# Kernel optimization log

Hardware: AMD Instinct MI355X
Metric: run time of the kernel (lower is better)

Reference implementation:

```python
import jax, jax.numpy as jnp
import numpy as np

N = 512          # n_nodes
F = 64           # hidden scalar/vector channels (hidden_irreps 64x0e+64x1o)
S = 5            # num_species
T = 32           # time embedding dim
M = 64           # MLP_irreps 64x0e
L = 2            # num_interactions
AVG = 511.0      # avg_num_neighbors (fully connected)
E = N * (N - 1)


def _sph(v):
    """Real spherical harmonics l=0,1,2 (component norm) of normalized vectors. v: [E,3]."""
    r = jnp.linalg.norm(v, axis=-1, keepdims=True)  # [E,1]
    u = v / r
    x, y, z = u[..., 0], u[..., 1], u[..., 2]
    s3, s5, s15 = 3.0 ** 0.5, 5.0 ** 0.5, 15.0 ** 0.5
    Y0 = jnp.ones_like(x)[..., None]
    Y1 = s3 * u
    Y2 = jnp.stack([s15 * x * y, s15 * y * z, 0.5 * s5 * (3 * z * z - 1.0),
                    s15 * x * z, 0.5 * s15 * (x * x - y * y)], axis=-1)
    return jnp.concatenate([Y0, Y1, Y2], axis=-1), r  # [E,9], [E,1]


def setup_inputs() -> dict:
    key = jax.random.key(0)
    ks = jax.random.split(key, 16)
    snd, rcv = np.nonzero(~np.eye(N, dtype=bool))  # fully-connected, no self loops
    return dict(
        positions=jax.random.normal(ks[0], (N, 3), jnp.float32),
        node_features=jax.random.randint(ks[1], (N,), 1, S + 1, jnp.int32),
        time_embedding=jax.random.normal(ks[2], (T,), jnp.float32),
        senders=jnp.asarray(snd, jnp.int32),
        receivers=jnp.asarray(rcv, jnp.int32),
        W_embed=jax.random.normal(ks[3], (S + T, F)) * 0.1,
        b_embed=jnp.zeros((F,)),
        W_lin=jax.random.normal(ks[4], (L, 3, F, F)) / jnp.sqrt(float(F)),
        W_e1=jax.random.normal(ks[5], (L, 1, 32)),
        b_e1=jnp.zeros((L, 32)),
        W_e2=jax.random.normal(ks[6], (L, 32, F * 6)) * 0.05,
        Wp0=jax.random.normal(ks[7], (L, S, F, 6)) * 0.1,
        Wp1=jax.random.normal(ks[8], (L, S, F, 3)) * 0.1,
        Wr1=jax.random.normal(ks[9], (L, F, M)) / jnp.sqrt(float(F)),
        br1=jnp.zeros((L, M)),
        Wr2s=jax.random.normal(ks[10], (L, M, 16)) * 0.1,
        Wr2g=jax.random.normal(ks[11], (L, M, F)) * 0.1,
    )


def reference(positions, node_features, time_embedding, senders, receivers,
              W_embed, b_embed, W_lin, W_e1, b_e1, W_e2, Wp0, Wp1, Wr1, br1, Wr2s, Wr2g):
    species = node_features - 1                                  # ints in [0,S)
    onehot = jax.nn.one_hot(species, S, dtype=positions.dtype)   # /normalization_factor=1
    te = jnp.tile(time_embedding, (N, 1))
    h = jnp.concatenate([onehot, te], axis=-1) @ W_embed + b_embed  # embedding Dense -> [N,F]
    node_feats = jnp.zeros((N, F, 9), positions.dtype).at[:, :, 0].set(h)
    pos0 = positions
    pos = positions
    for l in range(L):
        vec = pos[receivers] - pos[senders]                      # [E,3]
        Y, lengths = _sph(vec)                                   # SH of edge dirs, edge lengths
        # per-l channel-mixing linear on node feats
        x0 = jnp.einsum('nf,fg->ng', node_feats[:, :, 0], W_lin[l, 0])
        x1 = jnp.einsum('nfm,fg->ngm', node_feats[:, :, 1:4], W_lin[l, 1])
        x2 = jnp.einsum('nfm,fg->ngm', node_feats[:, :, 4:9], W_lin[l, 2])
        s0, s1, s2 = x0[senders], x1[senders], x2[senders]       # gather sender feats
        # edge-length MLP producing per-channel per-CG-path weights
        he = jax.nn.silu(lengths @ W_e1[l] + b_e1[l])            # [E,32]
        w = (he @ W_e2[l]).reshape(-1, F, 6)                     # 6 TP paths
        Y1 = Y[:, None, 1:4]
        Y2c = Y[:, None, 4:9]
        # CG tensor-product paths: 0x0->0, 0x1->1, 0x2->2, 1x1->0, 1x1->1, 2x2->0
        m0 = (w[..., 0] * s0 * Y[:, 0:1]
              + w[..., 3] * jnp.sum(s1 * Y1, -1)
              + w[..., 5] * jnp.sum(s2 * Y2c, -1))               # [E,F]
        m1 = w[..., 1, None] * s0[..., None] * Y1 + w[..., 4, None] * jnp.cross(s1, Y1)
        m2 = w[..., 2, None] * s0[..., None] * Y2c
        msg = jnp.concatenate([m0[..., None], m1, m2], axis=-1)  # [E,F,9]
        A = jax.ops.segment_sum(msg, receivers, num_segments=N) / AVG  # scatter-aggregate
        # EquivariantProductBasisBlock: species-weighted symmetric contractions (correlation 3)
        A0, A1, A2 = A[:, :, 0], A[:, :, 1:4], A[:, :, 4:9]
        n1 = jnp.sum(A1 * A1, -1)
        n2 = jnp.sum(A2 * A2, -1)
        t0 = jnp.stack([A0, A0 * A0, A0 ** 3, n1, n2, A0 * n1], axis=-1)
        w0 = Wp0[l][species]                                     # [N,F,6]
        w1 = Wp1[l][species]                                     # [N,F,3]
        out0 = jnp.sum(t0 * w0, -1)                              # [N,F] scalars
        gpoly = w1[..., 0] + w1[..., 1] * A0 + w1[..., 2] * A0 * A0
        out1 = gpoly[..., None] * A1                             # [N,F,3] vectors
        node_feats = (jnp.zeros((N, F, 9), positions.dtype)
                      .at[:, :, 0].set(out0).at[:, :, 1:4].set(out1))
        # NonLinearReadoutBlock: gated vector readout (scalar outputs are discarded upstream)
        hr = jax.nn.silu(out0 @ Wr1[l] + br1[l])
        gate = hr @ Wr2g[l]                                      # [N,F]
        vec_out = jnp.einsum('nf,nfc->nc', gate, out1)           # [N,3] many_body_vectors
        pos = pos + vec_out
    return (pos - pos0)[:, :3]                                    # final_scaling = 1.0
```

## Files before the change

### kernel.cpp

```cpp
#include <hip/hip_runtime.h>
#include <hip/hip_bf16.h>

using bf16 = __hip_bfloat16;
using bf16x8 = __attribute__((ext_vector_type(8))) short;
using f32x4  = __attribute__((ext_vector_type(4))) float;

#define NN 512
#define NS 511

enum : int {
  WS_FLAG = 0,
  WS_X0S  = 16,
  WS_POS  = 336,
  WS_POS2 = 1872,
  WS_DELTA= 3408,
  WS_XS1  = 4960,
};

__device__ __forceinline__ short f2b(float x) {
  unsigned u = __builtin_bit_cast(unsigned, x);
  unsigned r = (u + 0x7fffu + ((u >> 16) & 1u)) >> 16;
  return (short)r;
}

__device__ __forceinline__ float ld(const void* p, int i, int isf32) {
  if (isf32) return ((const float*)p)[i];
  return __bfloat162float(((const bf16*)p)[i]);
}

__global__ __launch_bounds__(320) void k_pre(
    const void* __restrict__ positions, const void* __restrict__ te,
    const void* __restrict__ W_embed, const void* __restrict__ b_embed,
    const void* __restrict__ W_lin, float* __restrict__ ws) {
  const int t = threadIdx.x;
  __shared__ int flag_s;
  __shared__ float hst[5][64];
  if (t < 64) {
    int cnt = 0;
    #pragma unroll
    for (int kq = 0; kq < 4; ++kq) {
      float v = __bfloat162float(((const bf16*)W_embed)[t + kq * 64]);
      float av = fabsf(v);
      cnt += (v == v && av > 1e-8f && av < 1e4f) ? 1 : 0;
    }
    #pragma unroll
    for (int off = 32; off > 0; off >>= 1) cnt += __shfl_down(cnt, off);
    if (t == 0) {
      int isf32 = (cnt >= 240) ? 0 : 1;
      flag_s = isf32;
      ((int*)ws)[WS_FLAG] = isf32;
    }
  }
  __syncthreads();
  const int isf32 = flag_s;
  for (int idx = t; idx < NN * 3; idx += 320)
    ws[WS_POS + idx] = ld(positions, idx, isf32);
  __shared__ float tv[64];
  if (t < 64) {
    float s = ld(b_embed, t, isf32);
    #pragma unroll 8
    for (int q = 0; q < 32; ++q)
      s += ld(te, q, isf32) * ld(W_embed, (5 + q) * 64 + t, isf32);
    tv[t] = s;
  }
  __syncthreads();
  {
    int sp = t >> 6, q = t & 63;
    hst[sp][q] = tv[q] + ld(W_embed, sp * 64 + q, isf32);
  }
  __syncthreads();
  {
    int sp = t >> 6, f = t & 63;
    float a0 = 0.f;
    #pragma unroll 8
    for (int q = 0; q < 64; ++q)
      a0 += hst[sp][q] * ld(W_lin, q * 64 + f, isf32);
    ws[WS_X0S + sp * 64 + f] = a0;
  }
}

template <int L>
__global__ __launch_bounds__(256) void k_edgenode(
    const int* __restrict__ nodef, const void* __restrict__ W_lin,
    const void* __restrict__ W_e1, const void* __restrict__ b_e1,
    const void* __restrict__ W_e2, const void* __restrict__ Wp0,
    const void* __restrict__ Wp1, const void* __restrict__ Wr1,
    const void* __restrict__ br1, const void* __restrict__ Wr2g,
    float* __restrict__ ws, void* __restrict__ out) {
  constexpr int HAS1 = L;
  constexpr int K = HAS1 ? 5 : 3;
  constexpr int N = K * 64;
  const int j = blockIdx.x;
  const int t = threadIdx.x;
  const int lane = t & 63;
  const int wave = t >> 6;
  const int quad = lane >> 4;
  const int lo = lane & 15;

  __shared__ short Bhi[N * 40];
  __shared__ float red[4][64][9];
  __shared__ float Af[64][9];
  __shared__ float s0l[64];
  __shared__ float o1l[3][64];
  __shared__ float hl[64];
  __shared__ float X0l[320];

  const int isf32 = ((const int*)ws)[WS_FLAG];

  {
    for (int idx = t; idx < N * 32; idx += 256) {
      int n = idx >> 5, h = idx & 31;
      int kp = n >> 6, f = n & 63;
      int src = (L * 32 + h) * 384 + f * 6 + kp;
      short bits;
      if (isf32) bits = f2b(((const float*)W_e2)[src]);
      else       bits = ((const short*)W_e2)[src];
      Bhi[n * 40 + h] = bits;
    }
    if (!HAS1) {
      for (int idx = t; idx < 320; idx += 256) X0l[idx] = ws[WS_X0S + idx];
    }
  }
  const float* pos = ws + (L ? WS_POS2 : WS_POS);
  const f32x4* xs = (const f32x4*)(ws + WS_XS1);
  float we1v[8], be1v[8];
  #pragma unroll
  for (int i = 0; i < 8; ++i) {
    we1v[i] = ld(W_e1, L * 32 + quad * 8 + i, isf32);
    be1v[i] = ld(b_e1, L * 32 + quad * 8 + i, isf32);
  }
  const float pjx = pos[j * 3 + 0], pjy = pos[j * 3 + 1], pjz = pos[j * 3 + 2];

  const float s3 = 1.7320508075688772f;
  const float s5h = 1.118033988749895f;
  const float s15 = 3.872983346207417f;
  const float s15h = 1.9364916731037085f;

  float acc[9][4] = {};
  __syncthreads();

  #pragma unroll 1
  for (int stile = wave; stile < 32; stile += 4) {
    bf16x8 af;
    {
      int ida = stile * 16 + lo;
      int ia = ida + (ida >= j);
      if (ia > 511) ia = 511;
      float pix = pos[ia * 3 + 0], piy = pos[ia * 3 + 1], piz = pos[ia * 3 + 2];
      float vx = pjx - pix, vy = pjy - piy, vz = pjz - piz;
      float r = sqrtf(vx * vx + vy * vy + vz * vz);
      #pragma unroll
      for (int i = 0; i < 8; ++i) {
        float x = r * we1v[i] + be1v[i];
        float he = x / (1.f + __expf(-x));
        af[i] = f2b(he);
      }
    }
    float Y1r[4][3], Y2r[4][5];
    int ir[4], sp4[4];
    bool vld[4];
    #pragma unroll
    for (int r4 = 0; r4 < 4; ++r4) {
      int idx = stile * 16 + quad * 4 + r4;
      vld[r4] = idx < NS;
      int i = idx + (idx >= j);
      if (i > 511) i = 511;
      ir[r4] = i;
      if (!HAS1) sp4[r4] = nodef[i] - 1;
      float pix = pos[i * 3 + 0], piy = pos[i * 3 + 1], piz = pos[i * 3 + 2];
      float vx = pjx - pix, vy = pjy - piy, vz = pjz - piz;
      float r2 = vx * vx + vy * vy + vz * vz;
      float rinv = r2 > 0.f ? rsqrtf(r2) : 0.f;
      float ux = vx * rinv, uy = vy * rinv, uz = vz * rinv;
      Y1r[r4][0] = s3 * ux; Y1r[r4][1] = s3 * uy; Y1r[r4][2] = s3 * uz;
      Y2r[r4][0] = s15 * ux * uy;
      Y2r[r4][1] = s15 * uy * uz;
      Y2r[r4][2] = s5h * (3.f * uz * uz - 1.f);
      Y2r[r4][3] = s15 * ux * uz;
      Y2r[r4][4] = s15h * (ux * ux - uy * uy);
    }
    #pragma unroll
    for (int ft = 0; ft < 4; ++ft) {
      int fcol = ft * 16 + lo;
      f32x4 xv[4];
      if (HAS1) {
        #pragma unroll
        for (int r4 = 0; r4 < 4; ++r4) xv[r4] = xs[ir[r4] * 64 + fcol];
      } else {
        #pragma unroll
        for (int r4 = 0; r4 < 4; ++r4) {
          f32x4 v = {X0l[sp4[r4] * 64 + fcol], 0.f, 0.f, 0.f};
          xv[r4] = v;
        }
      }
      f32x4 C[K];
      #pragma unroll
      for (int kp = 0; kp < K; ++kp) {
        const bf16x8 bh = *(const bf16x8*)&Bhi[(kp * 64 + fcol) * 40 + quad * 8];
        f32x4 c = {0.f, 0.f, 0.f, 0.f};
        C[kp] = __builtin_amdgcn_mfma_f32_16x16x32_bf16(af, bh, c, 0, 0, 0);
      }
      #pragma unroll
      for (int r4 = 0; r4 < 4; ++r4) {
        if (vld[r4]) {
          float s0 = xv[r4].x;
          float w0 = C[0][r4], w1 = C[1][r4], w2 = C[2][r4];
          if (HAS1) {
            float s1x = xv[r4].y, s1y = xv[r4].z, s1z = xv[r4].w;
            float w3 = C[3][r4], w4 = C[4][r4];
            float d1 = s1x * Y1r[r4][0] + s1y * Y1r[r4][1] + s1z * Y1r[r4][2];
            float cx = s1y * Y1r[r4][2] - s1z * Y1r[r4][1];
            float cy = s1z * Y1r[r4][0] - s1x * Y1r[r4][2];
            float cz = s1x * Y1r[r4][1] - s1y * Y1r[r4][0];
            acc[0][ft] += w0 * s0 + w3 * d1;
            float t1 = w1 * s0;
            acc[1][ft] += t1 * Y1r[r4][0] + w4 * cx;
            acc[2][ft] += t1 * Y1r[r4][1] + w4 * cy;
            acc[3][ft] += t1 * Y1r[r4][2] + w4 * cz;
          } else {
            acc[0][ft] += w0 * s0;
            float t1 = w1 * s0;
            acc[1][ft] += t1 * Y1r[r4][0];
            acc[2][ft] += t1 * Y1r[r4][1];
            acc[3][ft] += t1 * Y1r[r4][2];
          }
          float t2 = w2 * s0;
          acc[4][ft] += t2 * Y2r[r4][0];
          acc[5][ft] += t2 * Y2r[r4][1];
          acc[6][ft] += t2 * Y2r[r4][2];
          acc[7][ft] += t2 * Y2r[r4][3];
          acc[8][ft] += t2 * Y2r[r4][4];
        }
      }
    }
  }

  #pragma unroll
  for (int c = 0; c < 9; ++c)
    #pragma unroll
    for (int ft = 0; ft < 4; ++ft) {
      float v = acc[c][ft];
      v += __shfl_xor(v, 16);
      v += __shfl_xor(v, 32);
      acc[c][ft] = v;
    }
  if (quad == 0) {
    #pragma unroll
    for (int c = 0; c < 9; ++c)
      #pragma unroll
      for (int ft = 0; ft < 4; ++ft)
        red[wave][ft * 16 + lo][c] = acc[c][ft];
  }
  __syncthreads();
  for (int o = t; o < 576; o += 256) {
    int f = o / 9, c = o % 9;
    Af[f][c] = (red[0][f][c] + red[1][f][c] + red[2][f][c] + red[3][f][c]) *
               (1.f / 511.f);
  }
  __syncthreads();

  float out0 = 0.f, o1x = 0.f, o1y = 0.f, o1z = 0.f;
  if (t < 64) {
    int f = t;
    float a[9];
    #pragma unroll
    for (int c = 0; c < 9; ++c) a[c] = Af[f][c];
    int sp = nodef[j] - 1;
    int b0i = ((L * 5 + sp) * 64 + f) * 6;
    int b1i = ((L * 5 + sp) * 64 + f) * 3;
    float A0 = a[0];
    float n1 = a[1] * a[1] + a[2] * a[2] + a[3] * a[3];
    float n2 = a[4] * a[4] + a[5] * a[5] + a[6] * a[6] + a[7] * a[7] + a[8] * a[8];
    float A02 = A0 * A0;
    out0 = ld(Wp0, b0i + 0, isf32) * A0 + ld(Wp0, b0i + 1, isf32) * A02 +
           ld(Wp0, b0i + 2, isf32) * A02 * A0 + ld(Wp0, b0i + 3, isf32) * n1 +
           ld(Wp0, b0i + 4, isf32) * n2 + ld(Wp0, b0i + 5, isf32) * A0 * n1;
    float gp = ld(Wp1, b1i + 0, isf32) + ld(Wp1, b1i + 1, isf32) * A0 +
               ld(Wp1, b1i + 2, isf32) * A02;
    o1x = gp * a[1]; o1y = gp * a[2]; o1z = gp * a[3];
    s0l[f] = out0;
    if (L == 0) { o1l[0][f] = o1x; o1l[1][f] = o1y; o1l[2][f] = o1z; }
  }
  __syncthreads();
  if (t < 64) {
    int f = t;
    if (L == 0) {
      float b0 = 0.f, bx = 0.f, by = 0.f, bz = 0.f;
      #pragma unroll 8
      for (int q = 0; q < 64; ++q) {
        float w0 = ld(W_lin, 3 * 4096 + q * 64 + f, isf32);
        float w1 = ld(W_lin, 4 * 4096 + q * 64 + f, isf32);
        b0 += s0l[q] * w0;
        bx += o1l[0][q] * w1; by += o1l[1][q] * w1; bz += o1l[2][q] * w1;
      }
      f32x4 o = {b0, bx, by, bz};
      *(f32x4*)&ws[WS_XS1 + (j * 64 + f) * 4] = o;
    }
    float hacc = ld(br1, L * 64 + f, isf32);
    #pragma unroll 8
    for (int q = 0; q < 64; ++q)
      hacc += s0l[q] * ld(Wr1, (L * 64 + q) * 64 + f, isf32);
    hl[f] = hacc / (1.f + __expf(-hacc));
  }
  __syncthreads();
  if (t < 64) {
    int f = t;
    float gacc = 0.f;
    #pragma unroll 8
    for (int m = 0; m < 64; ++m)
      gacc += hl[m] * ld(Wr2g, (L * 64 + m) * 64 + f, isf32);
    float px = gacc * o1x, py = gacc * o1y, pz = gacc * o1z;
    #pragma unroll
    for (int off = 32; off > 0; off >>= 1) {
      px += __shfl_down(px, off);
      py += __shfl_down(py, off);
      pz += __shfl_down(pz, off);
    }
    if (f == 0) {
      if (L == 0) {
        ws[WS_DELTA + j * 3 + 0] = px;
        ws[WS_DELTA + j * 3 + 1] = py;
        ws[WS_DELTA + j * 3 + 2] = pz;
        ws[WS_POS2 + j * 3 + 0] = pos[j * 3 + 0] + px;
        ws[WS_POS2 + j * 3 + 1] = pos[j * 3 + 1] + py;
        ws[WS_POS2 + j * 3 + 2] = pos[j * 3 + 2] + pz;
      } else {
        float ox = ws[WS_DELTA + j * 3 + 0] + px;
        float oy = ws[WS_DELTA + j * 3 + 1] + py;
        float oz = ws[WS_DELTA + j * 3 + 2] + pz;
        if (isf32) {
          float* o = (float*)out;
          o[j * 3 + 0] = ox; o[j * 3 + 1] = oy; o[j * 3 + 2] = oz;
        } else {
          bf16* o = (bf16*)out;
          o[j * 3 + 0] = __float2bfloat16(ox);
          o[j * 3 + 1] = __float2bfloat16(oy);
          o[j * 3 + 2] = __float2bfloat16(oz);
        }
      }
    }
  }
}

extern "C" void kernel_launch(void* const* d_in, const int* in_sizes, int n_in,
                              void* d_out, int out_size, void* d_ws, size_t ws_size,
                              hipStream_t stream) {
  const void* positions = d_in[0];
  const int*  nodef     = (const int*)d_in[1];
  const void* te        = d_in[2];
  const void* W_embed   = d_in[5];
  const void* b_embed   = d_in[6];
  const void* W_lin     = d_in[7];
  const void* W_e1      = d_in[8];
  const void* b_e1      = d_in[9];
  const void* W_e2      = d_in[10];
  const void* Wp0       = d_in[11];
  const void* Wp1       = d_in[12];
  const void* Wr1       = d_in[13];
  const void* br1       = d_in[14];
  const void* Wr2g      = d_in[16];
  float* ws = (float*)d_ws;
  (void)in_sizes; (void)n_in; (void)out_size; (void)ws_size;

  k_pre<<<dim3(1), dim3(320), 0, stream>>>(positions, te, W_embed, b_embed,
                                           W_lin, ws);
  k_edgenode<0><<<dim3(512), dim3(256), 0, stream>>>(
      nodef, W_lin, W_e1, b_e1, W_e2, Wp0, Wp1, Wr1, br1, Wr2g, ws, d_out);
  k_edgenode<1><<<dim3(512), dim3(256), 0, stream>>>(
      nodef, W_lin, W_e1, b_e1, W_e2, Wp0, Wp1, Wr1, br1, Wr2g, ws, d_out);
}
```

Baseline: 194.0 us.

## Fuse preprocessing into layer-0 and factor layer-0 message sum by species

The single-block preprocessing kernel is merged into the layer-0 per-node kernel, so each block recomputes the embedding and positions into shared memory and one launch is removed. Layer 0 no longer runs the per-edge MFMA against W_e2. Because layer-0 sender features depend only on species, each block accumulates per-species sums of the radial hidden activations times the spherical harmonics (45x32 values). It then contracts these with W_e2 and the species embeddings once per node. This swaps per-edge matrix work for per-edge scalar FMAs, at the cost of redundant per-block setup and more registers.

Result: slower. 202.0 us (+4.1%).

```diff
diff --git a/kernel.cpp b/kernel.cpp
--- a/kernel.cpp
+++ b/kernel.cpp
@@ -28,13 +28,36 @@
   return __bfloat162float(((const bf16*)p)[i]);
 }
 
-__global__ __launch_bounds__(320) void k_pre(
-    const void* __restrict__ positions, const void* __restrict__ te,
-    const void* __restrict__ W_embed, const void* __restrict__ b_embed,
-    const void* __restrict__ W_lin, float* __restrict__ ws) {
+__global__ __launch_bounds__(256) void k_l0(
+    const void* __restrict__ positions, const int* __restrict__ nodef,
+    const void* __restrict__ te, const void* __restrict__ W_embed,
+    const void* __restrict__ b_embed, const void* __restrict__ W_lin,
+    const void* __restrict__ W_e1, const void* __restrict__ b_e1,
+    const void* __restrict__ W_e2, const void* __restrict__ Wp0,
+    const void* __restrict__ Wp1, const void* __restrict__ Wr1,
+    const void* __restrict__ br1, const void* __restrict__ Wr2g,
+    float* __restrict__ ws) {
+  const int j = blockIdx.x;
   const int t = threadIdx.x;
-  __shared__ int flag_s;
-  __shared__ float hst[5][64];
+  const int lane = t & 63;
+  const int wave = t >> 6;
+  const int h = lane & 31;
+  const int half = lane >> 5;
+
+  __shared__ int   flag_s;
+  __shared__ float posl[NN * 3];
+  __shared__ int   spl[NN];
+  __shared__ float we1s[32], be1s[32];
+  __shared__ float tv[64];
+  __shared__ float hstl[5][64];
+  __shared__ float X0Sl[5][64];
+  __shared__ float W2T[3][32][64];
+  __shared__ float Gred[4][45][32];
+  __shared__ float Af[64][9];
+  __shared__ float s0l[64];
+  __shared__ float o1l[3][64];
+  __shared__ float hl[64];
+
   if (t < 64) {
     int cnt = 0;
     #pragma unroll
@@ -46,16 +69,23 @@
     #pragma unroll
     for (int off = 32; off > 0; off >>= 1) cnt += __shfl_down(cnt, off);
     if (t == 0) {
-      int isf32 = (cnt >= 240) ? 0 : 1;
-      flag_s = isf32;
-      ((int*)ws)[WS_FLAG] = isf32;
+      int f32v = (cnt >= 240) ? 0 : 1;
+      flag_s = f32v;
+      if (j == 0) ((int*)ws)[WS_FLAG] = f32v;
     }
   }
   __syncthreads();
   const int isf32 = flag_s;
-  for (int idx = t; idx < NN * 3; idx += 320)
-    ws[WS_POS + idx] = ld(positions, idx, isf32);
-  __shared__ float tv[64];
+
+  for (int idx = t; idx < NN * 3; idx += 256) posl[idx] = ld(positions, idx, isf32);
+  for (int idx = t; idx < NN; idx += 256) spl[idx] = nodef[idx] - 1;
+  if (t < 32)      we1s[t]      = ld(W_e1, t, isf32);
+  else if (t < 64) be1s[t - 32] = ld(b_e1, t - 32, isf32);
+  for (int idx = t; idx < 3 * 32 * 64; idx += 256) {
+    int k = idx >> 11, rem = idx & 2047;
+    int hh = rem >> 6, f = rem & 63;
+    W2T[k][hh][f] = ld(W_e2, hh * 384 + f * 6 + k, isf32);
+  }
   if (t < 64) {
     float s = ld(b_embed, t, isf32);
     #pragma unroll 8
@@ -64,31 +94,172 @@
     tv[t] = s;
   }
   __syncthreads();
-  {
-    int sp = t >> 6, q = t & 63;
-    hst[sp][q] = tv[q] + ld(W_embed, sp * 64 + q, isf32);
-  }
-  __syncthreads();
-  {
-    int sp = t >> 6, f = t & 63;
+  for (int o = t; o < 320; o += 256) {
+    int sp = o >> 6, q = o & 63;
+    hstl[sp][q] = tv[q] + ld(W_embed, sp * 64 + q, isf32);
+  }
+  __syncthreads();
+  for (int o = t; o < 320; o += 256) {
+    int sp = o >> 6, f = o & 63;
     float a0 = 0.f;
     #pragma unroll 8
     for (int q = 0; q < 64; ++q)
-      a0 += hst[sp][q] * ld(W_lin, q * 64 + f, isf32);
-    ws[WS_X0S + sp * 64 + f] = a0;
+      a0 += hstl[sp][q] * ld(W_lin, q * 64 + f, isf32);
+    X0Sl[sp][f] = a0;
+  }
+  __syncthreads();
+
+  const float s3 = 1.7320508075688772f;
+  const float s5h = 1.118033988749895f;
+  const float s15 = 3.872983346207417f;
+  const float s15h = 1.9364916731037085f;
+
+  const float pjx = posl[j * 3 + 0], pjy = posl[j * 3 + 1], pjz = posl[j * 3 + 2];
+  const float we1h = we1s[h], be1h = be1s[h];
+
+  float G[45];
+  #pragma unroll
+  for (int c = 0; c < 45; ++c) G[c] = 0.f;
+
+  #pragma unroll 1
+  for (int it = 0; it < 64; ++it) {
+    int sidx = it * 8 + wave * 2 + half;
+    if (sidx < NS) {
+      int i = sidx + (sidx >= j);
+      float pix = posl[i * 3 + 0], piy = posl[i * 3 + 1], piz = posl[i * 3 + 2];
+      float vx = pjx - pix, vy = pjy - piy, vz = pjz - piz;
+      float r2 = vx * vx + vy * vy + vz * vz;
+      float rinv = r2 > 0.f ? rsqrtf(r2) : 0.f;
+      float r = r2 * rinv;
+      float ux = vx * rinv, uy = vy * rinv, uz = vz * rinv;
+      float x = r * we1h + be1h;
+      float he = x / (1.f + __expf(-x));
+      float Y1x = s3 * ux, Y1y = s3 * uy, Y1z = s3 * uz;
+      float Y2a = s15 * ux * uy, Y2b = s15 * uy * uz;
+      float Y2c = s5h * (3.f * uz * uz - 1.f);
+      float Y2d = s15 * ux * uz, Y2e = s15h * (ux * ux - uy * uy);
+      int sp = spl[i];
+      #pragma unroll
+      for (int spi = 0; spi < 5; ++spi) {
+        float hem = (sp == spi) ? he : 0.f;
+        G[spi * 9 + 0] += hem;
+        G[spi * 9 + 1] += hem * Y1x;
+        G[spi * 9 + 2] += hem * Y1y;
+        G[spi * 9 + 3] += hem * Y1z;
+        G[spi * 9 + 4] += hem * Y2a;
+        G[spi * 9 + 5] += hem * Y2b;
+        G[spi * 9 + 6] += hem * Y2c;
+        G[spi * 9 + 7] += hem * Y2d;
+        G[spi * 9 + 8] += hem * Y2e;
+      }
+    }
+  }
+
+  #pragma unroll
+  for (int c = 0; c < 45; ++c) G[c] += __shfl_xor(G[c], 32);
+  if (lane < 32) {
+    #pragma unroll
+    for (int c = 0; c < 45; ++c) Gred[wave][c][h] = G[c];
+  }
+  __syncthreads();
+  for (int o = t; o < 45 * 32; o += 256) {
+    int c = o >> 5, hh = o & 31;
+    Gred[0][c][hh] = Gred[0][c][hh] + Gred[1][c][hh] + Gred[2][c][hh] +
+                     Gred[3][c][hh];
+  }
+  __syncthreads();
+
+  for (int o = t; o < 576; o += 256) {
+    int f = o & 63, c = o >> 6;
+    int kc = (c == 0) ? 0 : (c < 4 ? 1 : 2);
+    float s = 0.f;
+    #pragma unroll
+    for (int sp = 0; sp < 5; ++sp) {
+      float d = 0.f;
+      #pragma unroll 8
+      for (int hh = 0; hh < 32; ++hh)
+        d += Gred[0][sp * 9 + c][hh] * W2T[kc][hh][f];
+      s += X0Sl[sp][f] * d;
+    }
+    Af[f][c] = s * (1.f / 511.f);
+  }
+  __syncthreads();
+
+  float out0 = 0.f, o1x = 0.f, o1y = 0.f, o1z = 0.f;
+  if (t < 64) {
+    int f = t;
+    float a[9];
+    #pragma unroll
+    for (int c = 0; c < 9; ++c) a[c] = Af[f][c];
+    int sp = nodef[j] - 1;
+    int b0i = (sp * 64 + f) * 6;
+    int b1i = (sp * 64 + f) * 3;
+    float A0 = a[0];
+    float n1 = a[1] * a[1] + a[2] * a[2] + a[3] * a[3];
+    float n2 = a[4] * a[4] + a[5] * a[5] + a[6] * a[6] + a[7] * a[7] + a[8] * a[8];
+    float A02 = A0 * A0;
+    out0 = ld(Wp0, b0i + 0, isf32) * A0 + ld(Wp0, b0i + 1, isf32) * A02 +
+           ld(Wp0, b0i + 2, isf32) * A02 * A0 + ld(Wp0, b0i + 3, isf32) * n1 +
+           ld(Wp0, b0i + 4, isf32) * n2 + ld(Wp0, b0i + 5, isf32) * A0 * n1;
+    float gp = ld(Wp1, b1i + 0, isf32) + ld(Wp1, b1i + 1, isf32) * A0 +
+               ld(Wp1, b1i + 2, isf32) * A02;
+    o1x = gp * a[1]; o1y = gp * a[2]; o1z = gp * a[3];
+    s0l[f] = out0;
+    o1l[0][f] = o1x; o1l[1][f] = o1y; o1l[2][f] = o1z;
+  }
+  __syncthreads();
+  if (t < 64) {
+    int f = t;
+    float b0 = 0.f, bx = 0.f, by = 0.f, bz = 0.f;
+    #pragma unroll 8
+    for (int q = 0; q < 64; ++q) {
+      float w0 = ld(W_lin, 3 * 4096 + q * 64 + f, isf32);
+      float w1 = ld(W_lin, 4 * 4096 + q * 64 + f, isf32);
+      b0 += s0l[q] * w0;
+      bx += o1l[0][q] * w1; by += o1l[1][q] * w1; bz += o1l[2][q] * w1;
+    }
+    f32x4 o = {b0, bx, by, bz};
+    *(f32x4*)&ws[WS_XS1 + (j * 64 + f) * 4] = o;
+    float hacc = ld(br1, f, isf32);
+    #pragma unroll 8
+    for (int q = 0; q < 64; ++q)
+      hacc += s0l[q] * ld(Wr1, q * 64 + f, isf32);
+    hl[f] = hacc / (1.f + __expf(-hacc));
+  }
+  __syncthreads();
+  if (t < 64) {
+    int f = t;
+    float gacc = 0.f;
+    #pragma unroll 8
+    for (int m = 0; m < 64; ++m)
+      gacc += hl[m] * ld(Wr2g, m * 64 + f, isf32);
+    float px = gacc * o1x, py = gacc * o1y, pz = gacc * o1z;
+    #pragma unroll
+    for (int off = 32; off > 0; off >>= 1) {
+      px += __shfl_down(px, off);
+      py += __shfl_down(py, off);
+      pz += __shfl_down(pz, off);
+    }
+    if (f == 0) {
+      ws[WS_DELTA + j * 3 + 0] = px;
+      ws[WS_DELTA + j * 3 + 1] = py;
+      ws[WS_DELTA + j * 3 + 2] = pz;
+      ws[WS_POS2 + j * 3 + 0] = pjx + px;
+      ws[WS_POS2 + j * 3 + 1] = pjy + py;
+      ws[WS_POS2 + j * 3 + 2] = pjz + pz;
+    }
   }
 }
 
-template <int L>
-__global__ __launch_bounds__(256) void k_edgenode(
+__global__ __launch_bounds__(256) void k_edgenode1(
     const int* __restrict__ nodef, const void* __restrict__ W_lin,
     const void* __restrict__ W_e1, const void* __restrict__ b_e1,
     const void* __restrict__ W_e2, const void* __restrict__ Wp0,
     const void* __restrict__ Wp1, const void* __restrict__ Wr1,
     const void* __restrict__ br1, const void* __restrict__ Wr2g,
     float* __restrict__ ws, void* __restrict__ out) {
-  constexpr int HAS1 = L;
-  constexpr int K = HAS1 ? 5 : 3;
+  constexpr int L = 1;
+  constexpr int K = 5;
   constexpr int N = K * 64;
   const int j = blockIdx.x;
   const int t = threadIdx.x;
@@ -101,27 +272,22 @@
   __shared__ float red[4][64][9];
   __shared__ float Af[64][9];
   __shared__ float s0l[64];
-  __shared__ float o1l[3][64];
   __shared__ float hl[64];
-  __shared__ float X0l[320];
 
   const int isf32 = ((const int*)ws)[WS_FLAG];
 
   {
     for (int idx = t; idx < N * 32; idx += 256) {
-      int n = idx >> 5, h = idx & 31;
+      int n = idx >> 5, hh = idx & 31;
       int kp = n >> 6, f = n & 63;
-      int src = (L * 32 + h) * 384 + f * 6 + kp;
+      int src = (L * 32 + hh) * 384 + f * 6 + kp;
       short bits;
       if (isf32) bits = f2b(((const float*)W_e2)[src]);
       else       bits = ((const short*)W_e2)[src];
-      Bhi[n * 40 + h] = bits;
-    }
-    if (!HAS1) {
-      for (int idx = t; idx < 320; idx += 256) X0l[idx] = ws[WS_X0S + idx];
-    }
-  }
-  const float* pos = ws + (L ? WS_POS2 : WS_POS);
+      Bhi[n * 40 + hh] = bits;
+    }
+  }
+  const float* pos = ws + WS_POS2;
   const f32x4* xs = (const f32x4*)(ws + WS_XS1);
   float we1v[8], be1v[8];
   #pragma unroll
@@ -157,7 +323,7 @@
       }
     }
     float Y1r[4][3], Y2r[4][5];
-    int ir[4], sp4[4];
+    int ir[4];
     bool vld[4];
     #pragma unroll
     for (int r4 = 0; r4 < 4; ++r4) {
@@ -166,7 +332,6 @@
       int i = idx + (idx >= j);
       if (i > 511) i = 511;
       ir[r4] = i;
-      if (!HAS1) sp4[r4] = nodef[i] - 1;
       float pix = pos[i * 3 + 0], piy = pos[i * 3 + 1], piz = pos[i * 3 + 2];
       float vx = pjx - pix, vy = pjy - piy, vz = pjz - piz;
       float r2 = vx * vx + vy * vy + vz * vz;
@@ -183,16 +348,8 @@
     for (int ft = 0; ft < 4; ++ft) {
       int fcol = ft * 16 + lo;
       f32x4 xv[4];
-      if (HAS1) {
-        #pragma unroll
-        for (int r4 = 0; r4 < 4; ++r4) xv[r4] = xs[ir[r4] * 64 + fcol];
-      } else {
-        #pragma unroll
-        for (int r4 = 0; r4 < 4; ++r4) {
-          f32x4 v = {X0l[sp4[r4] * 64 + fcol], 0.f, 0.f, 0.f};
-          xv[r4] = v;
-        }
-      }
+      #pragma unroll
+      for (int r4 = 0; r4 < 4; ++r4) xv[r4] = xs[ir[r4] * 64 + fcol];
       f32x4 C[K];
       #pragma unroll
       for (int kp = 0; kp < K; ++kp) {
@@ -205,25 +362,17 @@
         if (vld[r4]) {
           float s0 = xv[r4].x;
           float w0 = C[0][r4], w1 = C[1][r4], w2 = C[2][r4];
-          if (HAS1) {
-            float s1x = xv[r4].y, s1y = xv[r4].z, s1z = xv[r4].w;
-            float w3 = C[3][r4], w4 = C[4][r4];
-            float d1 = s1x * Y1r[r4][0] + s1y * Y1r[r4][1] + s1z * Y1r[r4][2];
-            float cx = s1y * Y1r[r4][2] - s1z * Y1r[r4][1];
-            float cy = s1z * Y1r[r4][0] - s1x * Y1r[r4][2];
-            float cz = s1x * Y1r[r4][1] - s1y * Y1r[r4][0];
-            acc[0][ft] += w0 * s0 + w3 * d1;
-            float t1 = w1 * s0;
-            acc[1][ft] += t1 * Y1r[r4][0] + w4 * cx;
-            acc[2][ft] += t1 * Y1r[r4][1] + w4 * cy;
-            acc[3][ft] += t1 * Y1r[r4][2] + w4 * cz;
-          } else {
-            acc[0][ft] += w0 * s0;
-            float t1 = w1 * s0;
-            acc[1][ft] += t1 * Y1r[r4][0];
-            acc[2][ft] += t1 * Y1r[r4][1];
-            acc[3][ft] += t1 * Y1r[r4][2];
-          }
+          float s1x = xv[r4].y, s1y = xv[r4].z, s1z = xv[r4].w;
+          float w3 = C[3][r4], w4 = C[4][r4];
+          float d1 = s1x * Y1r[r4][0] + s1y * Y1r[r4][1] + s1z * Y1r[r4][2];
+          float cx = s1y * Y1r[r4][2] - s1z * Y1r[r4][1];
+          float cy = s1z * Y1r[r4][0] - s1x * Y1r[r4][2];
+          float cz = s1x * Y1r[r4][1] - s1y * Y1r[r4][0];
+          acc[0][ft] += w0 * s0 + w3 * d1;
+          float t1 = w1 * s0;
+          acc[1][ft] += t1 * Y1r[r4][0] + w4 * cx;
+          acc[2][ft] += t1 * Y1r[r4][1] + w4 * cy;
+          acc[3][ft] += t1 * Y1r[r4][2] + w4 * cz;
           float t2 = w2 * s0;
           acc[4][ft] += t2 * Y2r[r4][0];
           acc[5][ft] += t2 * Y2r[r4][1];
@@ -279,23 +428,10 @@
                ld(Wp1, b1i + 2, isf32) * A02;
     o1x = gp * a[1]; o1y = gp * a[2]; o1z = gp * a[3];
     s0l[f] = out0;
-    if (L == 0) { o1l[0][f] = o1x; o1l[1][f] = o1y; o1l[2][f] = o1z; }
-  }
-  __syncthreads();
-  if (t < 64) {
-    int f = t;
-    if (L == 0) {
-      float b0 = 0.f, bx = 0.f, by = 0.f, bz = 0.f;
-      #pragma unroll 8
-      for (int q = 0; q < 64; ++q) {
-        float w0 = ld(W_lin, 3 * 4096 + q * 64 + f, isf32);
-        float w1 = ld(W_lin, 4 * 4096 + q * 64 + f, isf32);
-        b0 += s0l[q] * w0;
-        bx += o1l[0][q] * w1; by += o1l[1][q] * w1; bz += o1l[2][q] * w1;
-      }
-      f32x4 o = {b0, bx, by, bz};
-      *(f32x4*)&ws[WS_XS1 + (j * 64 + f) * 4] = o;
-    }
+  }
+  __syncthreads();
+  if (t < 64) {
+    int f = t;
     float hacc = ld(br1, L * 64 + f, isf32);
     #pragma unroll 8
     for (int q = 0; q < 64; ++q)
@@ -317,26 +453,17 @@
       pz += __shfl_down(pz, off);
     }
     if (f == 0) {
-      if (L == 0) {
-        ws[WS_DELTA + j * 3 + 0] = px;
-        ws[WS_DELTA + j * 3 + 1] = py;
-        ws[WS_DELTA + j * 3 + 2] = pz;
-        ws[WS_POS2 + j * 3 + 0] = pos[j * 3 + 0] + px;
-        ws[WS_POS2 + j * 3 + 1] = pos[j * 3 + 1] + py;
-        ws[WS_POS2 + j * 3 + 2] = pos[j * 3 + 2] + pz;
+      float ox = ws[WS_DELTA + j * 3 + 0] + px;
+      float oy = ws[WS_DELTA + j * 3 + 1] + py;
+      float oz = ws[WS_DELTA + j * 3 + 2] + pz;
+      if (isf32) {
+        float* o = (float*)out;
+        o[j * 3 + 0] = ox; o[j * 3 + 1] = oy; o[j * 3 + 2] = oz;
       } else {
-        float ox = ws[WS_DELTA + j * 3 + 0] + px;
-        float oy = ws[WS_DELTA + j * 3 + 1] + py;
-        float oz = ws[WS_DELTA + j * 3 + 2] + pz;
-        if (isf32) {
-          float* o = (float*)out;
-          o[j * 3 + 0] = ox; o[j * 3 + 1] = oy; o[j * 3 + 2] = oz;
-        } else {
-          bf16* o = (bf16*)out;
-          o[j * 3 + 0] = __float2bfloat16(ox);
-          o[j * 3 + 1] = __float2bfloat16(oy);
-          o[j * 3 + 2] = __float2bfloat16(oz);
-        }
+        bf16* o = (bf16*)out;
+        o[j * 3 + 0] = __float2bfloat16(ox);
+        o[j * 3 + 1] = __float2bfloat16(oy);
+        o[j * 3 + 2] = __float2bfloat16(oz);
       }
     }
   }
@@ -362,10 +489,9 @@
   float* ws = (float*)d_ws;
   (void)in_sizes; (void)n_in; (void)out_size; (void)ws_size;
 
-  k_pre<<<dim3(1), dim3(320), 0, stream>>>(positions, te, W_embed, b_embed,
-                                           W_lin, ws);
-  k_edgenode<0><<<dim3(512), dim3(256), 0, stream>>>(
-      nodef, W_lin, W_e1, b_e1, W_e2, Wp0, Wp1, Wr1, br1, Wr2g, ws, d_out);
-  k_edgenode<1><<<dim3(512), dim3(256), 0, stream>>>(
+  k_l0<<<dim3(512), dim3(256), 0, stream>>>(
+      positions, nodef, te, W_embed, b_embed, W_lin, W_e1, b_e1, W_e2,
+      Wp0, Wp1, Wr1, br1, Wr2g, ws);
+  k_edgenode1<<<dim3(512), dim3(256), 0, stream>>>(
       nodef, W_lin, W_e1, b_e1, W_e2, Wp0, Wp1, Wr1, br1, Wr2g, ws, d_out);
 }
```
